# Kernel optimization log

Measured on AMD Instinct MI355X. Metric: run time of the kernel, lower is better.

## Reference

```python
import jax, jax.numpy as jnp
import numpy as np

WS = 8  # window size (hardcoded in original forward)

def _window_partition(x, ws=WS):
    b, c, h, w = x.shape
    ph = (-h) % ws
    pw = (-w) % ws
    x = jnp.pad(x, ((0, 0), (0, 0), (0, ph), (0, pw)), mode='reflect')
    H, W = h + ph, w + pw
    # matches torch .view(b,c,ws,H//ws,ws,W//ws).permute(0,1,2,4,3,5)
    x = x.reshape(b, c, ws, H // ws, ws, W // ws)
    x = x.transpose(0, 1, 2, 4, 3, 5).reshape(b, c * ws * ws, H // ws, W // ws)
    return x, h, w, c, H // ws

def _l2norm_dim1(x):
    # F.normalize(x, p=2) defaults to dim=1 (token axis for [b, L, d]), eps=1e-12
    n = jnp.sqrt(jnp.sum(x * x, axis=1, keepdims=True))
    return x / jnp.maximum(n, 1e-12)

def _forward(q, k, v):
    b = q.shape[0]
    qp, qh, qw, qc, patch = _window_partition(q)
    kp, _, _, _, _ = _window_partition(k)
    vp, _, _, _, _ = _window_partition(v)
    d = qp.shape[1]  # c * ws * ws
    qt = qp.transpose(0, 2, 3, 1).reshape(b, -1, d)  # [b, L, d]
    kt = kp.transpose(0, 2, 3, 1).reshape(b, -1, d)
    vt = vp.transpose(0, 2, 3, 1).reshape(b, -1, d)
    _q = _l2norm_dim1(qt)
    _k = _l2norm_dim1(kt)
    _v = _l2norm_dim1(vt)
    sim = jnp.einsum('bld,bmd->blm', _q, _k) * (d ** -0.5)  # [b, L, L]
    out = jnp.einsum('blm,bmd->bld', jax.nn.softmax(sim, axis=-1), _v)
    # window_reverse
    L = out.shape[1]
    ws = WS
    x = out.reshape(b, patch, L // patch, qc, ws, ws)
    x = x.transpose(0, 3, 4, 1, 5, 2)  # (b, c, ws, patch, ws, L//patch)
    H = ws * patch
    x = x.reshape(b, qc, H, -1)
    return x[:, :, :qh, :qw]

def setup_inputs() -> dict:
    key = jax.random.key(0)
    kq, kk, kv = jax.random.split(key, 3)
    shape = (8, 32, 252, 252)
    return {
        'q': jax.random.normal(kq, shape, dtype=jnp.float32),
        'k': jax.random.normal(kk, shape, dtype=jnp.float32),
        'v': jax.random.normal(kv, shape, dtype=jnp.float32),
    }

def reference(q, k, v):
    return _forward(q, k, v)
```

## Files before the change

### kernel.cpp

```cpp
#include <hip/hip_runtime.h>
#include <cstdint>
#include <cstddef>


typedef __bf16 bf16x8 __attribute__((ext_vector_type(8)));
typedef float  f32x4  __attribute__((ext_vector_type(4)));

__device__ __forceinline__ unsigned int f2bf(float f) {
  unsigned int u = __builtin_bit_cast(unsigned int, f);
  u += 0x7FFFu + ((u >> 16) & 1u);
  return u >> 16;
}
__device__ __forceinline__ float bf2f(unsigned int h) {
  return __builtin_bit_cast(float, h << 16);
}

__device__ __forceinline__ void load_lds16(const void* g, void* l) {
  __builtin_amdgcn_global_load_lds(
      (const __attribute__((address_space(1))) void*)g,
      (__attribute__((address_space(3))) void*)l, 16, 0, 0);
}

__global__ __launch_bounds__(256)
void pack_qk_fused(const float* __restrict__ q, const float* __restrict__ k,
                   unsigned short* __restrict__ Qh,
                   unsigned short* __restrict__ Kh) {
  int bx  = blockIdx.x;
  int t   = bx >> 8;
  int b   = (bx >> 5) & 7;
  int i0  = (bx >> 2) & 7;
  int j0g = bx & 3;
  const float* xb = (t ? k : q) + (size_t)b * 32 * 63504;

  __shared__ float tf[32 * 65];
  __shared__ float red[512];
  __shared__ float sclt[64];

  int tid = threadIdx.x;
  int ch  = tid & 15;
  int c2  = tid >> 4;

  int wbase = j0g * 64 + ch * 4;
  float we[4];
  #pragma unroll
  for (int e = 0; e < 4; e++) {
    int w = wbase + e;
    we[e] = (w >= 252) ? 0.f : (((unsigned)(w - 247) <= 3u) ? 2.f : 1.f);
  }
  bool tail = (wbase == 252);

  float pa = 0.f, pb = 0.f;
  unsigned short* X = (t ? Kh : Qh) + (size_t)b * 1024 * 2048;

  int gsub = tid & 7;
  int gj1  = tid >> 3;
  int gjl  = gsub >> 2;
  int gc0  = (gsub & 3) * 8;

  for (int i1 = 0; i1 < 32; i1++) {
    int h  = i0 * 32 + i1;
    int hs = (h < 252) ? h : 502 - h;
    float rw = (h >= 252) ? 0.f : (((unsigned)(h - 247) <= 3u) ? 2.f : 1.f);
    const float* rowp = xb + (size_t)hs * 252;

    #pragma unroll
    for (int it = 0; it < 2; it++) {
      int c = c2 + it * 16;
      const float* src = rowp + (size_t)c * 63504;
      float4 vv;
      if (!tail) {
        vv = *(const float4*)&src[wbase];
      } else {
        vv.x = src[250]; vv.y = src[249]; vv.z = src[248]; vv.w = src[247];
      }
      float s = rw * (we[0] * vv.x * vv.x + we[1] * vv.y * vv.y +
                      we[2] * vv.z * vv.z + we[3] * vv.w * vv.w);
      if (it == 0) pa += s; else pb += s;
      float* dst = &tf[c * 65 + ch * 4];
      dst[0] = vv.x; dst[1] = vv.y; dst[2] = vv.z; dst[3] = vv.w;
    }
    __syncthreads();
    {
      int pos = gjl * 32 + gj1;
      unsigned int ov[4];
      #pragma unroll
      for (int m = 0; m < 4; m++) {
        unsigned int lo = f2bf(tf[(gc0 + 2 * m)     * 65 + pos]);
        unsigned int hi = f2bf(tf[(gc0 + 2 * m + 1) * 65 + pos]);
        ov[m] = lo | (hi << 16);
      }
      int l = i1 * 32 + gj1;
      uint4 o4; o4.x = ov[0]; o4.y = ov[1]; o4.z = ov[2]; o4.w = ov[3];
      *(uint4*)&X[(size_t)l * 2048 + i0 * 256 + j0g * 64 + gsub * 8] = o4;
    }
    __syncthreads();
  }

  red[tid] = pa; red[256 + tid] = pb;
  __syncthreads();
  if (tid < 64) {
    int c = tid & 31, jl = tid >> 5;
    int base = (c & 15) * 16 + jl * 8 + ((c >= 16) ? 256 : 0);
    float s = 0.f;
    #pragma unroll
    for (int u = 0; u < 8; u++) s += red[base + u];
    sclt[c * 2 + jl] = 1.f / fmaxf(sqrtf(s), 1e-12f);
  }
  __syncthreads();

  {
    float sc[8];
    #pragma unroll
    for (int m = 0; m < 8; m++) sc[m] = sclt[(gc0 + m) * 2 + gjl];
    unsigned short* basep = &X[i0 * 256 + j0g * 64 + gsub * 8];
    int lb = tid >> 3;
    #pragma unroll 4
    for (int it = 0; it < 32; it++) {
      size_t off = (size_t)(it * 32 + lb) * 2048;
      uint4 u = *(uint4*)&basep[off];
      uint4 o;
      o.x = f2bf(bf2f(u.x & 0xFFFF) * sc[0]) | (f2bf(bf2f(u.x >> 16) * sc[1]) << 16);
      o.y = f2bf(bf2f(u.y & 0xFFFF) * sc[2]) | (f2bf(bf2f(u.y >> 16) * sc[3]) << 16);
      o.z = f2bf(bf2f(u.z & 0xFFFF) * sc[4]) | (f2bf(bf2f(u.z >> 16) * sc[5]) << 16);
      o.w = f2bf(bf2f(u.w & 0xFFFF) * sc[6]) | (f2bf(bf2f(u.w >> 16) * sc[7]) << 16);
      *(uint4*)&basep[off] = o;
    }
  }
}

__global__ void pack_v_kernel(const float* __restrict__ v,
                              unsigned short* __restrict__ Vt,
                              float* __restrict__ svsum) {
  int bx = blockIdx.x;
  int b  = bx >> 8;
  int i0 = (bx >> 5) & 7;
  int i1 = bx & 31;
  int h  = i0 * 32 + i1;
  int hs = (h < 252) ? h : 502 - h;
  const float* src = v + (size_t)b * 32 * 63504 + (size_t)hs * 252;
  unsigned short* dst = Vt + (size_t)b * 2048 * 1024
                           + (size_t)(i0 * 256) * 1024 + i1 * 32;

  int tid = threadIdx.x;
  int j1c = tid & 3;
  int c   = (tid >> 2) & 31;
  int j0g = tid >> 7;
  const float* s = src + (size_t)c * 63504;

  float psum[4];

  #pragma unroll
  for (int jj = 0; jj < 4; jj++) {
    int j0 = j0g * 4 + jj;
    int w0 = j0 * 32 + j1c * 8;
    float f0, f1, f2, f3, f4, f5, f6, f7;
    if (w0 + 8 <= 252) {
      float4 a = *(const float4*)&s[w0];
      float4 bq = *(const float4*)&s[w0 + 4];
      f0 = a.x; f1 = a.y; f2 = a.z; f3 = a.w;
      f4 = bq.x; f5 = bq.y; f6 = bq.z; f7 = bq.w;
    } else {
      float4 a = *(const float4*)&s[244];
      float4 bq = *(const float4*)&s[248];
      f0 = bq.x; f1 = bq.y; f2 = bq.z; f3 = bq.w;
      f4 = bq.z; f5 = bq.y; f6 = bq.x; f7 = a.w;
    }
    psum[jj] = f0*f0 + f1*f1 + f2*f2 + f3*f3 + f4*f4 + f5*f5 + f6*f6 + f7*f7;
    uint4 o;
    o.x = f2bf(f0) | (f2bf(f1) << 16);
    o.y = f2bf(f2) | (f2bf(f3) << 16);
    o.z = f2bf(f4) | (f2bf(f5) << 16);
    o.w = f2bf(f6) | (f2bf(f7) << 16);
    *(uint4*)&dst[(size_t)(j0 * 32 + c) * 1024 + j1c * 8] = o;
  }

  #pragma unroll
  for (int jj = 0; jj < 4; jj++) {
    float ssum = psum[jj];
    ssum += __shfl_down(ssum, 2, 4);
    ssum += __shfl_down(ssum, 1, 4);
    if (j1c == 0) {
      int j0 = j0g * 4 + jj;
      atomicAdd(&svsum[(size_t)b * 2048 + i0 * 256 + j0 * 32 + c], ssum);
    }
  }
}

template <int MODE>
__global__ __launch_bounds__(256, 4)
void gemm_nt(const unsigned short* __restrict__ A,
             const unsigned short* __restrict__ B,
             int K, int Asb, int Bsb, void* __restrict__ Cout, float scale,
             const float* __restrict__ sv) {
  __shared__ unsigned short lA[128 * 64];
  __shared__ unsigned short lB[128 * 64];
  __shared__ float svb[(MODE == 1) ? 128 : 1];

  const int flat = blockIdx.x;
  const int zz   = flat & 7;
  const int rr   = flat >> 3;
  const int my   = rr >> 3;
  const int nx   = rr & 7;

  const int tid  = threadIdx.x;
  const int lane = tid & 63;
  const int wave = tid >> 6;
  const int ln15 = lane & 15;
  const int q4   = lane >> 4;
  const int wm   = wave >> 1;
  const int wn   = wave & 1;
  const int m0   = my * 128;
  const int n0   = nx * 128;
  const unsigned short* Ab = A + (size_t)zz * Asb;
  const unsigned short* Bb = B + (size_t)zz * Bsb;

  if (MODE == 1 && tid < 128)
    svb[tid] = 1.f / fmaxf(sqrtf(sv[(size_t)zz * 2048 + m0 + tid]), 1e-12f);

  const int srow = lane >> 3;
  const int kcp  = lane & 7;
  const int kcl  = kcp ^ srow;

  f32x4 acc[4][4] = {};

  for (int k0 = 0; k0 < K; k0 += 64) {
    #pragma unroll
    for (int r = 0; r < 4; r++) {
      int rowg = wave * 32 + r * 8;
      int row  = rowg + srow;
      load_lds16(&Ab[(size_t)(m0 + row) * K + k0 + kcl * 8], &lA[rowg * 64]);
      load_lds16(&Bb[(size_t)(n0 + row) * K + k0 + kcl * 8], &lB[rowg * 64]);
    }
    __syncthreads();
    #pragma unroll
    for (int kk = 0; kk < 2; kk++) {
      bf16x8 af[4], bfr[4];
      #pragma unroll
      for (int mt = 0; mt < 4; mt++) {
        int row = wm * 64 + mt * 16 + ln15;
        int pc  = (kk * 4 + q4) ^ (row & 7);
        af[mt] = *(const bf16x8*)&lA[row * 64 + pc * 8];
      }
      #pragma unroll
      for (int nt = 0; nt < 4; nt++) {
        int row = wn * 64 + nt * 16 + ln15;
        int pc  = (kk * 4 + q4) ^ (row & 7);
        bfr[nt] = *(const bf16x8*)&lB[row * 64 + pc * 8];
      }
      #pragma unroll
      for (int mt = 0; mt < 4; mt++)
        #pragma unroll
        for (int nt = 0; nt < 4; nt++)
          acc[mt][nt] = __builtin_amdgcn_mfma_f32_16x16x32_bf16(
              af[mt], bfr[nt], acc[mt][nt], 0, 0, 0);
    }
    __syncthreads();
  }

  if (MODE == 0) {
    unsigned short* Sb = (unsigned short*)Cout + (size_t)zz * 1024 * 1024;
    #pragma unroll
    for (int mt = 0; mt < 4; mt++) {
      #pragma unroll
      for (int nt = 0; nt < 4; nt++) {
        int col = n0 + wn * 64 + nt * 16 + ln15;
        #pragma unroll
        for (int rg = 0; rg < 4; rg++) {
          int rowi = m0 + wm * 64 + mt * 16 + q4 * 4 + rg;
          Sb[(size_t)rowi * 1024 + col] = (unsigned short)f2bf(acc[mt][nt][rg] * scale);
        }
      }
    }
  } else {
    float* Ob = (float*)Cout;
    #pragma unroll
    for (int mt = 0; mt < 4; mt++) {
      #pragma unroll
      for (int nt = 0; nt < 4; nt++) {
        int l  = n0 + wn * 64 + nt * 16 + ln15;
        int i1 = l >> 5, j1 = l & 31;
        #pragma unroll
        for (int rg = 0; rg < 4; rg++) {
          int rloc = wm * 64 + mt * 16 + q4 * 4 + rg;
          int dp = m0 + rloc;
          int c  = dp & 31;
          int j0 = (dp >> 5) & 7;
          int i0 = dp >> 8;
          int h = i0 * 32 + i1;
          int w = j0 * 32 + j1;
          if (h < 252 && w < 252)
            Ob[(((size_t)zz * 32 + c) * 252 + h) * 252 + w] =
                acc[mt][nt][rg] * svb[rloc];
        }
      }
    }
  }
}

__global__ void softmax_kernel(unsigned short* __restrict__ S) {
  unsigned short* row = S + (size_t)blockIdx.x * 1024;
  int tid  = threadIdx.x;
  int lane = tid & 63;
  int wid  = tid >> 6;

  uint2 u = *(const uint2*)&row[tid * 4];
  float x0 = bf2f(u.x & 0xFFFF);
  float x1 = bf2f(u.x >> 16);
  float x2 = bf2f(u.y & 0xFFFF);
  float x3 = bf2f(u.y >> 16);

  __shared__ float red[8];
  float mx = fmaxf(fmaxf(x0, x1), fmaxf(x2, x3));
  #pragma unroll
  for (int off = 32; off > 0; off >>= 1) mx = fmaxf(mx, __shfl_down(mx, off));
  if (lane == 0) red[wid] = mx;
  __syncthreads();
  if (tid == 0)
    red[4] = fmaxf(fmaxf(red[0], red[1]), fmaxf(red[2], red[3]));
  __syncthreads();
  float bm = red[4];

  float e0 = __expf(x0 - bm), e1 = __expf(x1 - bm);
  float e2 = __expf(x2 - bm), e3 = __expf(x3 - bm);
  float s = e0 + e1 + e2 + e3;
  #pragma unroll
  for (int off = 32; off > 0; off >>= 1) s += __shfl_down(s, off);
  if (lane == 0) red[wid] = s;
  __syncthreads();
  if (tid == 0) red[5] = 1.0f / (red[0] + red[1] + red[2] + red[3]);
  __syncthreads();
  float inv = red[5];

  unsigned int o0 = f2bf(e0 * inv) | (f2bf(e1 * inv) << 16);
  unsigned int o1 = f2bf(e2 * inv) | (f2bf(e3 * inv) << 16);
  uint2 o; o.x = o0; o.y = o1;
  *(uint2*)&row[tid * 4] = o;
}

extern "C" void kernel_launch(void* const* d_in, const int* in_sizes, int n_in,
                              void* d_out, int out_size, void* d_ws, size_t ws_size,
                              hipStream_t stream) {
  const float* q = (const float*)d_in[0];
  const float* k = (const float*)d_in[1];
  const float* v = (const float*)d_in[2];
  float* out = (float*)d_out;

  char* ws = (char*)d_ws;
  float* sv = (float*)ws;
  unsigned short* Qh = (unsigned short*)(ws + 196608);
  unsigned short* Kh = Qh + (size_t)8 * 1024 * 2048;
  unsigned short* Vt = Kh + (size_t)8 * 1024 * 2048;
  unsigned short* S  = Vt + (size_t)8 * 2048 * 1024;

  const float SIM_SCALE = 0.02209708691207961f;

  hipMemsetAsync(sv, 0, (size_t)8 * 2048 * sizeof(float), stream);
  pack_qk_fused<<<512, 256, 0, stream>>>(q, k, Qh, Kh);
  pack_v_kernel<<<2048, 256, 0, stream>>>(v, Vt, sv);
  gemm_nt<0><<<512, 256, 0, stream>>>(
      Qh, Kh, 2048, 1024 * 2048, 1024 * 2048, (void*)S, SIM_SCALE, nullptr);
  softmax_kernel<<<8192, 256, 0, stream>>>(S);
  gemm_nt<1><<<1024, 256, 0, stream>>>(
      Vt, S, 1024, 2048 * 1024, 1024 * 1024, (void*)out, 1.0f, sv);
}
```

Baseline: 378.5 us.

## Pipeline pack_qk input rows through async global-to-LDS loads with 4-deep buffering

Rewrites the Q/K packing kernel so each input row is fetched with global_load_lds directly into one of four LDS buffers, with three rows prefetched ahead and explicit vmcnt waits plus barriers. The reflect-pad tail is handled by loading an aligned chunk and remapping the token position, and the sum-of-squares for normalization moves into the consumer phase with per-thread accumulators and a wider reduction. The aim is to overlap global memory latency with the bf16 conversion and stores, at the cost of more LDS and hand-counted waitcnt values that must match the number of outstanding memory operations, including the stores.

```diff
diff --git a/kernel.cpp b/kernel.cpp
--- a/kernel.cpp
+++ b/kernel.cpp
@@ -20,6 +20,8 @@
       (const __attribute__((address_space(1))) void*)g,
       (__attribute__((address_space(3))) void*)l, 16, 0, 0);
 }
+
+#define WAITV(n) asm volatile("s_waitcnt vmcnt(" #n ")" ::: "memory")
 
 __global__ __launch_bounds__(256)
 void pack_qk_fused(const float* __restrict__ q, const float* __restrict__ k,
@@ -32,24 +34,16 @@
   int j0g = bx & 3;
   const float* xb = (t ? k : q) + (size_t)b * 32 * 63504;
 
-  __shared__ float tf[32 * 65];
-  __shared__ float red[512];
+  __shared__ float tf[4][2048];
+  __shared__ float red[2048];
   __shared__ float sclt[64];
 
-  int tid = threadIdx.x;
-  int ch  = tid & 15;
-  int c2  = tid >> 4;
-
-  int wbase = j0g * 64 + ch * 4;
-  float we[4];
-  #pragma unroll
-  for (int e = 0; e < 4; e++) {
-    int w = wbase + e;
-    we[e] = (w >= 252) ? 0.f : (((unsigned)(w - 247) <= 3u) ? 2.f : 1.f);
-  }
-  bool tail = (wbase == 252);
-
-  float pa = 0.f, pb = 0.f;
+  int tid   = threadIdx.x;
+  int wave  = tid >> 6;
+  int lane  = tid & 63;
+  int lquad = lane >> 4;
+  int lpos  = (lane & 15) * 4;
+
   unsigned short* X = (t ? Kh : Qh) + (size_t)b * 1024 * 2048;
 
   int gsub = tid & 7;
@@ -57,53 +51,77 @@
   int gjl  = gsub >> 2;
   int gc0  = (gsub & 3) * 8;
 
-  for (int i1 = 0; i1 < 32; i1++) {
+  int pos_tok = gjl * 32 + gj1;
+  int w_tok   = j0g * 64 + pos_tok;
+  int pos_r   = (w_tok < 252) ? pos_tok : 118 - pos_tok;
+  float wt    = (w_tok >= 252) ? 0.f
+              : (((unsigned)(w_tok - 247) <= 3u) ? 2.f : 1.f);
+
+  bool clampw = (j0g == 3) && (lpos == 60);
+  int  wsrc   = clampw ? 236 : (j0g * 64 + lpos);
+
+  auto stage_issue = [&](int i1, int buf) {
     int h  = i0 * 32 + i1;
     int hs = (h < 252) ? h : 502 - h;
-    float rw = (h >= 252) ? 0.f : (((unsigned)(h - 247) <= 3u) ? 2.f : 1.f);
-    const float* rowp = xb + (size_t)hs * 252;
-
-    #pragma unroll
-    for (int it = 0; it < 2; it++) {
-      int c = c2 + it * 16;
-      const float* src = rowp + (size_t)c * 63504;
-      float4 vv;
-      if (!tail) {
-        vv = *(const float4*)&src[wbase];
-      } else {
-        vv.x = src[250]; vv.y = src[249]; vv.z = src[248]; vv.w = src[247];
-      }
-      float s = rw * (we[0] * vv.x * vv.x + we[1] * vv.y * vv.y +
-                      we[2] * vv.z * vv.z + we[3] * vv.w * vv.w);
-      if (it == 0) pa += s; else pb += s;
-      float* dst = &tf[c * 65 + ch * 4];
-      dst[0] = vv.x; dst[1] = vv.y; dst[2] = vv.z; dst[3] = vv.w;
-    }
-    __syncthreads();
-    {
-      int pos = gjl * 32 + gj1;
-      unsigned int ov[4];
-      #pragma unroll
-      for (int m = 0; m < 4; m++) {
-        unsigned int lo = f2bf(tf[(gc0 + 2 * m)     * 65 + pos]);
-        unsigned int hi = f2bf(tf[(gc0 + 2 * m + 1) * 65 + pos]);
-        ov[m] = lo | (hi << 16);
-      }
-      int l = i1 * 32 + gj1;
-      uint4 o4; o4.x = ov[0]; o4.y = ov[1]; o4.z = ov[2]; o4.w = ov[3];
-      *(uint4*)&X[(size_t)l * 2048 + i0 * 256 + j0g * 64 + gsub * 8] = o4;
-    }
-    __syncthreads();
-  }
-
-  red[tid] = pa; red[256 + tid] = pb;
+    const float* rowp = xb + (size_t)hs * 252 + wsrc;
+    #pragma unroll
+    for (int j = 0; j < 2; j++) {
+      int seg = wave * 2 + j;
+      int c   = seg * 4 + lquad;
+      load_lds16(rowp + (size_t)c * 63504, &tf[buf][seg * 256]);
+    }
+  };
+
+  float pa[8] = {0.f, 0.f, 0.f, 0.f, 0.f, 0.f, 0.f, 0.f};
+
+  stage_issue(0, 0);
+  stage_issue(1, 1);
+  stage_issue(2, 2);
+
+  for (int i1 = 0; i1 < 32; i1++) {
+    if (i1 < 29) stage_issue(i1 + 3, (i1 + 3) & 3);
+
+    if      (i1 == 0)  WAITV(6);
+    else if (i1 == 1)  WAITV(7);
+    else if (i1 == 2)  WAITV(8);
+    else if (i1 < 29)  WAITV(9);
+    else if (i1 == 29) WAITV(7);
+    else if (i1 == 30) WAITV(5);
+    else               WAITV(3);
+    __builtin_amdgcn_s_barrier();
+
+    int h  = i0 * 32 + i1;
+    float rw  = (h >= 252) ? 0.f : (((unsigned)(h - 247) <= 3u) ? 2.f : 1.f);
+    float rwt = rw * wt;
+
+    const float* tb = tf[i1 & 3];
+    unsigned int ov[4];
+    #pragma unroll
+    for (int m = 0; m < 4; m++) {
+      float x0 = tb[(gc0 + 2 * m)     * 64 + pos_r];
+      float x1 = tb[(gc0 + 2 * m + 1) * 64 + pos_r];
+      pa[2 * m]     += rwt * x0 * x0;
+      pa[2 * m + 1] += rwt * x1 * x1;
+      ov[m] = f2bf(x0) | (f2bf(x1) << 16);
+    }
+    int l = i1 * 32 + gj1;
+    uint4 o4; o4.x = ov[0]; o4.y = ov[1]; o4.z = ov[2]; o4.w = ov[3];
+    *(uint4*)&X[(size_t)l * 2048 + i0 * 256 + j0g * 64 + gsub * 8] = o4;
+
+    __builtin_amdgcn_s_barrier();
+  }
+
+  __syncthreads();
+  #pragma unroll
+  for (int e = 0; e < 8; e++) red[e * 256 + tid] = pa[e];
   __syncthreads();
   if (tid < 64) {
     int c = tid & 31, jl = tid >> 5;
-    int base = (c & 15) * 16 + jl * 8 + ((c >= 16) ? 256 : 0);
+    int gs = jl * 4 + (c >> 3);
+    int e  = c & 7;
     float s = 0.f;
     #pragma unroll
-    for (int u = 0; u < 8; u++) s += red[base + u];
+    for (int g = 0; g < 32; g++) s += red[e * 256 + g * 8 + gs];
     sclt[c * 2 + jl] = 1.f / fmaxf(sqrtf(s), 1e-12f);
   }
   __syncthreads();
```

Result: faster. 358.3 us (-5.3%).

## Stage whole Q/K pack tile in LDS to avoid global read-modify-write pass

Applied to the files above, without the earlier changes.

The fused Q/K pack kernel used to write unscaled bf16 rows to global memory every row iteration and then reread and rescale them in global memory once the norms were known. Now the block keeps its entire 1024x64 bf16 tile in a large padded LDS buffer, drops the per-row barriers, and writes the normalized output to global memory only once. This removes a full global read and write of Qh/Kh, but uses about 139KB of LDS per block, which limits occupancy, and the final stores shrink to 8-byte chunks.

```diff
diff --git a/kernel.cpp b/kernel.cpp
--- a/kernel.cpp
+++ b/kernel.cpp
@@ -32,7 +32,7 @@
   int j0g = bx & 3;
   const float* xb = (t ? k : q) + (size_t)b * 32 * 63504;
 
-  __shared__ float tf[32 * 65];
+  __shared__ unsigned short tile[1024 * 68];
   __shared__ float red[512];
   __shared__ float sclt[64];
 
@@ -52,16 +52,15 @@
   float pa = 0.f, pb = 0.f;
   unsigned short* X = (t ? Kh : Qh) + (size_t)b * 1024 * 2048;
 
-  int gsub = tid & 7;
-  int gj1  = tid >> 3;
-  int gjl  = gsub >> 2;
-  int gc0  = (gsub & 3) * 8;
+  int j0l  = ch >> 3;
+  int j1b  = (ch * 4) & 31;
 
   for (int i1 = 0; i1 < 32; i1++) {
     int h  = i0 * 32 + i1;
     int hs = (h < 252) ? h : 502 - h;
     float rw = (h >= 252) ? 0.f : (((unsigned)(h - 247) <= 3u) ? 2.f : 1.f);
     const float* rowp = xb + (size_t)hs * 252;
+    int lbase = i1 * 32 + j1b;
 
     #pragma unroll
     for (int it = 0; it < 2; it++) {
@@ -76,25 +75,15 @@
       float s = rw * (we[0] * vv.x * vv.x + we[1] * vv.y * vv.y +
                       we[2] * vv.z * vv.z + we[3] * vv.w * vv.w);
       if (it == 0) pa += s; else pb += s;
-      float* dst = &tf[c * 65 + ch * 4];
-      dst[0] = vv.x; dst[1] = vv.y; dst[2] = vv.z; dst[3] = vv.w;
-    }
-    __syncthreads();
-    {
-      int pos = gjl * 32 + gj1;
-      unsigned int ov[4];
-      #pragma unroll
-      for (int m = 0; m < 4; m++) {
-        unsigned int lo = f2bf(tf[(gc0 + 2 * m)     * 65 + pos]);
-        unsigned int hi = f2bf(tf[(gc0 + 2 * m + 1) * 65 + pos]);
-        ov[m] = lo | (hi << 16);
-      }
-      int l = i1 * 32 + gj1;
-      uint4 o4; o4.x = ov[0]; o4.y = ov[1]; o4.z = ov[2]; o4.w = ov[3];
-      *(uint4*)&X[(size_t)l * 2048 + i0 * 256 + j0g * 64 + gsub * 8] = o4;
-    }
-    __syncthreads();
-  }
+      int o = j0l * 32 + c;
+      unsigned short* tp = &tile[(size_t)lbase * 68 + o];
+      tp[0]   = (unsigned short)f2bf(vv.x);
+      tp[68]  = (unsigned short)f2bf(vv.y);
+      tp[136] = (unsigned short)f2bf(vv.z);
+      tp[204] = (unsigned short)f2bf(vv.w);
+    }
+  }
+  __syncthreads();
 
   red[tid] = pa; red[256 + tid] = pb;
   __syncthreads();
@@ -104,26 +93,27 @@
     float s = 0.f;
     #pragma unroll
     for (int u = 0; u < 8; u++) s += red[base + u];
-    sclt[c * 2 + jl] = 1.f / fmaxf(sqrtf(s), 1e-12f);
+    sclt[jl * 32 + c] = 1.f / fmaxf(sqrtf(s), 1e-12f);
   }
   __syncthreads();
 
   {
-    float sc[8];
-    #pragma unroll
-    for (int m = 0; m < 8; m++) sc[m] = sclt[(gc0 + m) * 2 + gjl];
-    unsigned short* basep = &X[i0 * 256 + j0g * 64 + gsub * 8];
-    int lb = tid >> 3;
+    int qd = tid & 15;
+    int lr = tid >> 4;
+    float sc[4];
+    #pragma unroll
+    for (int m = 0; m < 4; m++) sc[m] = sclt[qd * 4 + m];
+    unsigned short* Xb = &X[i0 * 256 + j0g * 64 + qd * 4];
     #pragma unroll 4
-    for (int it = 0; it < 32; it++) {
-      size_t off = (size_t)(it * 32 + lb) * 2048;
-      uint4 u = *(uint4*)&basep[off];
-      uint4 o;
-      o.x = f2bf(bf2f(u.x & 0xFFFF) * sc[0]) | (f2bf(bf2f(u.x >> 16) * sc[1]) << 16);
-      o.y = f2bf(bf2f(u.y & 0xFFFF) * sc[2]) | (f2bf(bf2f(u.y >> 16) * sc[3]) << 16);
-      o.z = f2bf(bf2f(u.z & 0xFFFF) * sc[4]) | (f2bf(bf2f(u.z >> 16) * sc[5]) << 16);
-      o.w = f2bf(bf2f(u.w & 0xFFFF) * sc[6]) | (f2bf(bf2f(u.w >> 16) * sc[7]) << 16);
-      *(uint4*)&basep[off] = o;
+    for (int it = 0; it < 64; it++) {
+      int l = it * 16 + lr;
+      uint2 u = *(const uint2*)&tile[(size_t)l * 68 + qd * 4];
+      uint2 o2;
+      o2.x = f2bf(bf2f(u.x & 0xFFFF) * sc[0]) |
+             (f2bf(bf2f(u.x >> 16)   * sc[1]) << 16);
+      o2.y = f2bf(bf2f(u.y & 0xFFFF) * sc[2]) |
+             (f2bf(bf2f(u.y >> 16)   * sc[3]) << 16);
+      *(uint2*)&Xb[(size_t)l * 2048] = o2;
     }
   }
 }
```

Result: slower. 405.1 us (+7.0%).
